# Performance work log

Hardware: AMD Instinct MI355X
Metric: run time of the kernel (lower is better)

## Reference

```python
import jax, jax.numpy as jnp
import numpy as np

DIM = 64

def conv2d_g2(x, w, b):
    # 3x3 conv, padding=1, groups=2, NCHW
    y = jax.lax.conv_general_dilated(x, w, (1, 1), [(1, 1), (1, 1)],
                                     dimension_numbers=('NCHW', 'OIHW', 'NCHW'),
                                     feature_group_count=2)
    return y + b[None, :, None, None]

def bilinear_gather(x, py, px):
    # x: [B,C,H,W]; py,px: [B,K,H,W] float sample coords -> [B,K,H,W,C]
    B, C, H, W = x.shape
    y0 = jnp.floor(py); x0 = jnp.floor(px)
    ly = py - y0; lx = px - x0
    hy = 1.0 - ly; hx = 1.0 - lx
    b_idx = jnp.arange(B)[:, None, None, None]
    def gather(yi, xi):
        valid = (yi >= 0) & (yi < H) & (xi >= 0) & (xi < W)
        yc = jnp.clip(yi, 0, H - 1).astype(jnp.int32)
        xc = jnp.clip(xi, 0, W - 1).astype(jnp.int32)
        v = x[b_idx, :, yc, xc]  # [B,K,H,W,C]
        return v * valid[..., None].astype(x.dtype)
    return (gather(y0, x0) * (hy * hx)[..., None]
            + gather(y0, x0 + 1) * (hy * lx)[..., None]
            + gather(y0 + 1, x0) * (ly * hx)[..., None]
            + gather(y0 + 1, x0 + 1) * (ly * lx)[..., None])

def deform_dw(x, offset, w, b, k, pad, dil):
    # depthwise (groups=C, offset_groups=1) deformable conv, stride 1
    B, C, H, W = x.shape
    K = k * k
    off = offset.reshape(B, K, 2, H, W)  # torchvision layout: (dy,dx) per kernel tap
    ky = jnp.repeat(jnp.arange(k), k).astype(x.dtype)   # [K]
    kx = jnp.tile(jnp.arange(k), k).astype(x.dtype)     # [K]
    base_y = jnp.arange(H, dtype=x.dtype)[None, None, :, None] - pad + dil * ky[None, :, None, None]
    base_x = jnp.arange(W, dtype=x.dtype)[None, None, None, :] - pad + dil * kx[None, :, None, None]
    py = base_y + off[:, :, 0]  # [B,K,H,W]
    px = base_x + off[:, :, 1]
    val = bilinear_gather(x, py, px)  # [B,K,H,W,C]
    return jnp.einsum('bkhwc,ck->bchw', val, w.reshape(C, K)) + b[None, :, None, None]

def lsk_forward(x, w_off3, b_off3, w_off2, b_off2, w7, b7, w5, b5):
    B, C, H, W = x.shape
    offset3 = conv2d_g2(x, w_off3, b_off3)            # [B,98,H,W]
    out1 = deform_dw(x, offset3, w7, b7, 7, 9, 3)     # [B,C,H,W]
    offset2 = conv2d_g2(x, w_off2, b_off2)            # [B,50,H,W]
    out2 = deform_dw(out1, offset2, w5, b5, 5, 6, 3)  # [B,C,H,W]
    feats = jnp.stack([out1, out2], axis=1)           # [B,2,C,H,W]
    gap = feats.mean(axis=(3, 4), keepdims=True)      # [B,2,C,1,1]
    attn = jax.nn.softmax(gap, axis=1)
    return jnp.sum(feats * attn, axis=1)              # [B,C,H,W]

def setup_inputs() -> dict:
    key = jax.random.key(0)
    ks = jax.random.split(key, 9)
    B, C, H, W = 4, DIM, 56, 56
    return {
        'x':      jax.random.normal(ks[0], (B, C, H, W), jnp.float32),
        'w_off3': jax.random.normal(ks[1], (98, C // 2, 3, 3), jnp.float32) * 0.05,
        'b_off3': jax.random.normal(ks[2], (98,), jnp.float32) * 0.05,
        'w_off2': jax.random.normal(ks[3], (50, C // 2, 3, 3), jnp.float32) * 0.05,
        'b_off2': jax.random.normal(ks[4], (50,), jnp.float32) * 0.05,
        'w7':     jax.random.normal(ks[5], (C, 1, 7, 7), jnp.float32) * 0.1,
        'b7':     jax.random.normal(ks[6], (C,), jnp.float32) * 0.05,
        'w5':     jax.random.normal(ks[7], (C, 1, 5, 5), jnp.float32) * 0.1,
        'b5':     jax.random.normal(ks[8], (C,), jnp.float32) * 0.05,
    }

def reference(x, w_off3, b_off3, w_off2, b_off2, w7, b7, w5, b5):
    return lsk_forward(x, w_off3, b_off3, w_off2, b_off2, w7, b7, w5, b5)
```

## Files before the change

### kernel.cpp

```cpp
#include <hip/hip_runtime.h>
#include <hip/hip_fp16.h>
#include <math.h>

#define HH 56
#define WW 56
#define CC 64
#define BB 4
#define HWA (HH*WW)

typedef _Float16 half8_t __attribute__((ext_vector_type(8)));
typedef _Float16 h2_t   __attribute__((ext_vector_type(2)));
typedef float f32x4_t __attribute__((ext_vector_type(4)));

#define PROWS 57
#define PSTRB (PROWS*57*64*4)
#define ROWSTRB (57*64*4)

__global__ __launch_bounds__(256)
void k_prep(const float* __restrict__ x,
            const float* __restrict__ w3, const float* __restrict__ w2,
            const float* __restrict__ b3, const float* __restrict__ b2,
            __half2* __restrict__ xp, _Float16* __restrict__ xh,
            _Float16* __restrict__ Wp, float* __restrict__ bbp) {
    int blk = blockIdx.x;
    int tid = threadIdx.x;
    if (blk < BB*56) {
        __shared__ float ld[64*57];
        int b = blk / 56, y = blk % 56;
        for (int i = tid; i < 64*56; i += 256) {
            int c = i / 56, col = i % 56;
            ld[c*57 + col] = x[((size_t)b*CC + c)*HWA + y*WW + col];
        }
        __syncthreads();
        for (int i = tid; i < 57*64; i += 256) {
            int j = i >> 6, c = i & 63;
            float lo = (j > 0)  ? ld[c*57 + j - 1] : 0.f;
            float hi = (j < 56) ? ld[c*57 + j]     : 0.f;
            xp[((size_t)(b*PROWS + y)*57 + j)*CC + c] = __floats2half2_rn(lo, hi);
        }
        _Float16* dst = xh + (((size_t)(b*2)*56 + y)*58)*32;
        for (int i = tid; i < 2*58*32; i += 256) {
            int g = i / 1856;
            int r = i % 1856;
            int col = r / 32, ic = r % 32;
            float v = 0.f;
            if (col >= 1 && col <= 56) v = ld[(g*32 + ic)*57 + col - 1];
            dst[(size_t)g*56*58*32 + r] = (_Float16)v;
        }
    } else {
        int i = (blk - BB*56)*256 + tid;
        if (i < 46080) {
            int j    = i & 7;
            int lane = (i >> 3) & 63;
            int mt   = (i >> 9) % 5;
            int kt   = (i / 2560) % 9;
            int g    = i / 23040;
            int m  = mt*16 + (lane & 15);
            int ic = (lane >> 4)*8 + j;
            int ky = kt/3, kx = kt%3;
            float v = 0.f;
            if (m < 49)      v = w3[((g*49 + m)*32 + ic)*9 + ky*3 + kx];
            else if (m < 74) v = w2[((g*25 + (m-49))*32 + ic)*9 + ky*3 + kx];
            Wp[i] = (_Float16)v;
        } else if (i < 46240) {
            int t = i - 46080; int g = t/80, m = t%80;
            float v = 0.f;
            if (m < 49)      v = b3[g*49 + m];
            else if (m < 74) v = b2[g*25 + (m-49)];
            bbp[t] = v;
        }
    }
}

__global__ __launch_bounds__(256)
void k_convmfma(const _Float16* __restrict__ xh, const _Float16* __restrict__ Wp,
                const float* __restrict__ bb,
                float* __restrict__ off3, float* __restrict__ off2) {
    __shared__ _Float16 tile[4][3*18*32];
    int blk = blockIdx.x;
    int iy = blk % 56;
    int g  = (blk / 56) & 1;
    int b  = blk / 112;
    int wv   = threadIdx.y;
    int lane = threadIdx.x;
    int n0 = wv * 16;

    const unsigned int* xs = (const unsigned int*)xh;
    unsigned int* tl = (unsigned int*)&tile[wv][0];
#pragma unroll
    for (int i = 0; i < 14; ++i) {
        int idx = i*64 + lane;
        if (idx < 864) {
            int ic2 = idx & 15;
            int seg = idx >> 4;
            int cl = seg % 18, r = seg / 18;
            int y = iy - 1 + r, col = n0 + cl;
            unsigned int v = 0;
            if (y >= 0 && y < 56 && col < 58)
                v = xs[(((size_t)(b*2+g)*56 + y)*58 + col)*16 + ic2];
            tl[idx] = v;
        }
    }
    __syncthreads();

    int nlo = lane & 15, khi = lane >> 4;
    f32x4_t acc[5];
#pragma unroll
    for (int mt = 0; mt < 5; ++mt) acc[mt] = (f32x4_t){0.f,0.f,0.f,0.f};

    const half8_t* wp8 = (const half8_t*)Wp;
#pragma unroll
    for (int kt = 0; kt < 9; ++kt) {
        int ky = kt/3, kx = kt%3;
        half8_t bfrag = *(const half8_t*)&tile[wv][((ky*18) + nlo + kx)*32 + khi*8];
#pragma unroll
        for (int mt = 0; mt < 5; ++mt) {
            half8_t afrag = wp8[(((size_t)g*9 + kt)*5 + mt)*64 + lane];
            acc[mt] = __builtin_amdgcn_mfma_f32_16x16x32_f16(afrag, bfrag, acc[mt], 0, 0, 0);
        }
    }

    int pixcol = n0 + nlo;
    if (pixcol < 56) {
        int pix = iy*WW + pixcol;
#pragma unroll
        for (int mt = 0; mt < 5; ++mt) {
#pragma unroll
            for (int r = 0; r < 4; ++r) {
                int m = mt*16 + khi*4 + r;
                if (m < 74) {
                    float val = acc[mt][r] + bb[g*80 + m];
                    if (m < 49)
                        off3[((size_t)b*98 + g*49 + m)*HWA + pix] = val;
                    else
                        off2[((size_t)b*50 + g*25 + (m-49))*HWA + pix] = val;
                }
            }
        }
    }
}

template<int K, int KS, int PAD, bool WP>
__global__ __launch_bounds__(256)
void k_deform(const _Float16* __restrict__ xp, const float* __restrict__ off,
              const float* __restrict__ wg, const float* __restrict__ bias,
              float* __restrict__ out, float* __restrict__ partial,
              _Float16* __restrict__ xpo) {
    __shared__ float lw[K*65];
    __shared__ float loffs[2*K][9];
    __shared__ float red[8][64];
    int tid = threadIdx.x + threadIdx.y*64;
    int blk = blockIdx.x;
    int xcd = blk & 7;
    int idx = blk >> 3;
    int b   = xcd >> 1;
    int hw0 = (xcd & 1)*(HWA/2) + idx*8;

    for (int i = tid; i < K*64; i += 256) {
        int c = i / K, t = i % K;
        lw[t*65 + c] = wg[i];
    }
    for (int i = tid; i < 4*K; i += 256) {
        int row = i >> 1, half = i & 1;
        float4 v = *(const float4*)&off[((size_t)b*2*K + row)*HWA + hw0 + half*4];
        loffs[row][half*4 + 0] = v.x; loffs[row][half*4 + 1] = v.y;
        loffs[row][half*4 + 2] = v.z; loffs[row][half*4 + 3] = v.w;
    }
    __syncthreads();

    int yp = threadIdx.y;
    int c  = threadIdx.x;

    int mx0 = 0, wz0 = 0, ww0 = 0;
    int mx1 = 0, wz1 = 0, ww1 = 0;
    if (c < K) {
        int t = c;
        int ky = t / KS, kx = t % KS;
#pragma unroll
        for (int s = 0; s < 2; ++s) {
            int p = yp + 4*s;
            int hw = hw0 + p;
            int h = hw / WW, w = hw % WW;
            float py = (float)(h - PAD + 3*ky) + loffs[2*t][p];
            float px = (float)(w - PAD + 3*kx) + loffs[2*t+1][p];
            float y0f = floorf(py), x0f = floorf(px);
            float ly = py - y0f, lx = px - x0f;
            float hy = 1.f - ly, hx = 1.f - lx;
            int y0 = (int)y0f, x0 = (int)x0f;
            int j = x0 + 1;
            bool jv = (j >= 0) && (j <= 56);
            int jc = jv ? j : 0;
            float s0 = ((y0   >= 0) && (y0   < HH) && jv) ? hy : 0.f;
            float s1 = ((y0+1 >= 0) && (y0+1 < HH) && jv) ? ly : 0.f;
            bool use1 = (s0 == 0.f);
            int rbase = use1 ? min(max(y0 + 1, 0), 55) : y0;
            float aw = use1 ? s1 : s0;
            float bw = use1 ? 0.f : s1;
            int mxv = (rbase*57 + jc)*(64*4);
            __half2 wah = __floats2half2_rn(aw*hx, aw*lx);
            __half2 wbh = __floats2half2_rn(bw*hx, bw*lx);
            if (s == 0) { mx0 = mxv; wz0 = *(int*)&wah; ww0 = *(int*)&wbh; }
            else        { mx1 = mxv; wz1 = *(int*)&wah; ww1 = *(int*)&wbh; }
        }
    }

    const char* xb = (const char*)xp + (size_t)b*PSTRB;
    float acc0 = 0.f, acc1 = 0.f;
#pragma unroll 4
    for (int t = 0; t < K; ++t) {
        int m0 = (int)__builtin_amdgcn_readlane(mx0, t);
        int z0 = (int)__builtin_amdgcn_readlane(wz0, t);
        int w0 = (int)__builtin_amdgcn_readlane(ww0, t);
        int m1 = (int)__builtin_amdgcn_readlane(mx1, t);
        int z1 = (int)__builtin_amdgcn_readlane(wz1, t);
        int w1 = (int)__builtin_amdgcn_readlane(ww1, t);
        const h2_t* r0p = (const h2_t*)(xb + m0);
        const h2_t* r1p = (const h2_t*)(xb + m0 + ROWSTRB);
        const h2_t* r2p = (const h2_t*)(xb + m1);
        const h2_t* r3p = (const h2_t*)(xb + m1 + ROWSTRB);
        h2_t r0a = r0p[c];
        h2_t r1a = r1p[c];
        h2_t r0b = r2p[c];
        h2_t r1b = r3p[c];
        float lwv = lw[t*65 + c];
        float v0 = __builtin_amdgcn_fdot2(r0a, *(h2_t*)&z0, 0.f, false);
        v0 = __builtin_amdgcn_fdot2(r1a, *(h2_t*)&w0, v0, false);
        float v1 = __builtin_amdgcn_fdot2(r0b, *(h2_t*)&z1, 0.f, false);
        v1 = __builtin_amdgcn_fdot2(r1b, *(h2_t*)&w1, v1, false);
        acc0 = fmaf(v0, lwv, acc0);
        acc1 = fmaf(v1, lwv, acc1);
    }
    float bs = bias[c];
    float val0 = acc0 + bs;
    float val1 = acc1 + bs;
    int hwA = hw0 + yp, hwB = hw0 + yp + 4;
    out[((size_t)b*HWA + hwA)*CC + c] = val0;
    out[((size_t)b*HWA + hwB)*CC + c] = val1;

    if (WP) {
#pragma unroll
        for (int s = 0; s < 2; ++s) {
            int hw = s ? hwB : hwA;
            float val = s ? val1 : val0;
            int y = hw / WW, w = hw % WW;
            _Float16* base = xpo + ((size_t)(b*PROWS + y)*57)*CC*2;
            _Float16 hv = (_Float16)val;
            base[((w    )*64 + c)*2 + 1] = hv;
            base[((w + 1)*64 + c)*2 + 0] = hv;
            if (w == 0)  base[(c)*2 + 0] = (_Float16)0.f;
            if (w == 55) base[((56)*64 + c)*2 + 1] = (_Float16)0.f;
        }
    }

    red[yp][c] = val0;
    red[yp + 4][c] = val1;
    __syncthreads();
    if (yp == 0) {
        float s = red[0][c] + red[1][c] + red[2][c] + red[3][c]
                + red[4][c] + red[5][c] + red[6][c] + red[7][c];
        partial[((size_t)b*(HWA/8) + (hw0 >> 3))*64 + c] = s;
    }
}

__global__ void k_gapA(const float* __restrict__ p1, const float* __restrict__ p2,
                       float* __restrict__ g2) {
    __shared__ float red[4][64];
    int blk = blockIdx.x;
    int chunk = blk % 14;
    int bf    = blk / 14;
    int b     = bf >> 1;
    const float* p = (bf & 1) ? p2 : p1;
    int tid = threadIdx.x;
    int c = tid & 63, s = tid >> 6;
    float sum = 0.f;
#pragma unroll
    for (int i = 0; i < 7; ++i) {
        int j = chunk*28 + s + 4*i;
        sum += p[((size_t)b*(HWA/8) + j)*64 + c];
    }
    red[s][c] = sum;
    __syncthreads();
    if (s == 0)
        g2[((size_t)bf*14 + chunk)*64 + c]
            = red[0][c] + red[1][c] + red[2][c] + red[3][c];
}

__global__ void k_combine(const float* __restrict__ o1, const float* __restrict__ o2,
                          const float* __restrict__ g2, float* __restrict__ out) {
    __shared__ float tile[64][65];
    __shared__ float gsh[2][64];
    int blk = blockIdx.x;
    int b   = blk / (HWA/64);
    int t0  = (blk % (HWA/64)) * 64;
    int tid = threadIdx.x;
    int c = tid & 63, q = tid >> 6;

    if (tid < 128) {
        int f = tid >> 6, cc = tid & 63;
        float s = 0.f;
#pragma unroll
        for (int k = 0; k < 14; ++k)
            s += g2[((size_t)(b*2+f)*14 + k)*64 + cc];
        gsh[f][cc] = s * (1.f/HWA);
    }
    __syncthreads();

    float g1v = gsh[0][c];
    float g2v = gsh[1][c];
    float m  = fmaxf(g1v, g2v);
    float e1 = expf(g1v - m), e2 = expf(g2v - m);
    float a1 = e1 / (e1 + e2), a2 = 1.f - a1;

#pragma unroll
    for (int i = 0; i < 16; ++i) {
        int p = q + 4*i;
        size_t idx = ((size_t)b*HWA + t0 + p)*CC + c;
        tile[p][c] = o1[idx]*a1 + o2[idx]*a2;
    }
    __syncthreads();
    int p2 = tid & 63;
#pragma unroll
    for (int i = 0; i < 16; ++i) {
        int c2 = q + 4*i;
        out[((size_t)b*CC + c2)*HWA + t0 + p2] = tile[p2][c2];
    }
}

extern "C" void kernel_launch(void* const* d_in, const int* in_sizes, int n_in,
                              void* d_out, int out_size, void* d_ws, size_t ws_size,
                              hipStream_t stream) {
    const float* x      = (const float*)d_in[0];
    const float* w_off3 = (const float*)d_in[1];
    const float* b_off3 = (const float*)d_in[2];
    const float* w_off2 = (const float*)d_in[3];
    const float* b_off2 = (const float*)d_in[4];
    const float* w7     = (const float*)d_in[5];
    const float* b7     = (const float*)d_in[6];
    const float* w5     = (const float*)d_in[7];
    const float* b5     = (const float*)d_in[8];
    float* out = (float*)d_out;

    const size_t PAIRF = (size_t)BB*PROWS*57*64;
    float* ws    = (float*)d_ws;
    float* off3r = ws;
    float* off2r = off3r + 1229312;
    float* out1  = off2r + 627200;
    float* out2  = out1  + 802816;
    float* xp1f  = out2  + 802816;
    float* xp2f  = xp1f  + PAIRF;
    float* xhf   = xp2f  + PAIRF;
    float* part1 = xhf   + 415744;
    float* part2 = part1 + 100352;
    float* gpA   = part2 + 100352;
    float* wpf   = gpA   + 7168;
    float* bbp   = wpf   + 23040;
    __half2*  xp1 = (__half2*)xp1f;
    _Float16* xp2h = (_Float16*)xp2f;
    _Float16* xh  = (_Float16*)xhf;
    _Float16* Wp  = (_Float16*)wpf;
    size_t need = (size_t)(1229312 + 627200 + 802816*2 + 831744*2 + 415744
                           + 100352*2 + 7168 + 23040 + 160) * 4;
    if (ws_size < need) return;

    k_prep<<<BB*56 + 181, 256, 0, stream>>>(x, w_off3, w_off2, b_off3, b_off2,
                                            xp1, xh, Wp, bbp);
    k_convmfma<<<BB*2*56, dim3(64,4), 0, stream>>>(xh, Wp, bbp, off3r, off2r);
    k_deform<49,7,9,true><<<BB*(HWA/8), dim3(64,4), 0, stream>>>(
        (const _Float16*)xp1, off3r, w7, b7, out1, part1, xp2h);
    k_deform<25,5,6,false><<<BB*(HWA/8), dim3(64,4), 0, stream>>>(
        xp2h, off2r, w5, b5, out2, part2, nullptr);
    k_gapA<<<8*14, 256, 0, stream>>>(part1, part2, gpA);
    k_combine<<<BB*(HWA/64), 256, 0, stream>>>(out1, out2, gpA, out);
}
```

Measured before the change: 139.6 us.

## Vectorize conv tile loads and combine reads, deepen deform loop unroll

The MFMA conv kernel now fills its shared tile with 16-byte uint4 loads instead of 4-byte loads. The combine kernel computes the softmax attention weights once per channel and reads o1/o2 as float4. The deformable-conv tap loop is unrolled by 8 instead of 4, and the prep kernel's fp16 repack loop is split per group so it uses shifts instead of div/mod. These changes aim to cut memory instruction count and integer overhead, at the cost of possible register pressure from the deeper unroll and more LDS bank conflicts on the strided tile writes.

After: 135.2 us (median of 3 runs). 1.03x faster.

```diff
diff --git a/kernel.cpp b/kernel.cpp
--- a/kernel.cpp
+++ b/kernel.cpp
@@ -39,13 +39,13 @@
             xp[((size_t)(b*PROWS + y)*57 + j)*CC + c] = __floats2half2_rn(lo, hi);
         }
         _Float16* dst = xh + (((size_t)(b*2)*56 + y)*58)*32;
-        for (int i = tid; i < 2*58*32; i += 256) {
-            int g = i / 1856;
-            int r = i % 1856;
-            int col = r / 32, ic = r % 32;
-            float v = 0.f;
-            if (col >= 1 && col <= 56) v = ld[(g*32 + ic)*57 + col - 1];
-            dst[(size_t)g*56*58*32 + r] = (_Float16)v;
+#pragma unroll
+        for (int g = 0; g < 2; ++g) {
+            for (int i = tid; i < 1856; i += 256) {
+                int col = i >> 5, ic = i & 31;
+                float v = (col >= 1 && col <= 56) ? ld[(g*32 + ic)*57 + col - 1] : 0.f;
+                dst[(size_t)g*(56*58*32) + i] = (_Float16)v;
+            }
         }
     } else {
         int i = (blk - BB*56)*256 + tid;
@@ -85,20 +85,20 @@
     int lane = threadIdx.x;
     int n0 = wv * 16;
 
-    const unsigned int* xs = (const unsigned int*)xh;
-    unsigned int* tl = (unsigned int*)&tile[wv][0];
-#pragma unroll
-    for (int i = 0; i < 14; ++i) {
-        int idx = i*64 + lane;
-        if (idx < 864) {
-            int ic2 = idx & 15;
-            int seg = idx >> 4;
+    const uint4* xs4 = (const uint4*)xh;
+    uint4* tl4 = (uint4*)&tile[wv][0];
+#pragma unroll
+    for (int i = 0; i < 4; ++i) {
+        int idx4 = i*64 + lane;
+        if (idx4 < 216) {
+            int ic4 = idx4 & 3;
+            int seg = idx4 >> 2;
             int cl = seg % 18, r = seg / 18;
             int y = iy - 1 + r, col = n0 + cl;
-            unsigned int v = 0;
+            uint4 v = {0u, 0u, 0u, 0u};
             if (y >= 0 && y < 56 && col < 58)
-                v = xs[(((size_t)(b*2+g)*56 + y)*58 + col)*16 + ic2];
-            tl[idx] = v;
+                v = xs4[((((size_t)(b*2+g)*56 + y)*58 + col) << 2) + ic4];
+            tl4[idx4] = v;
         }
     }
     __syncthreads();
@@ -206,7 +206,7 @@
 
     const char* xb = (const char*)xp + (size_t)b*PSTRB;
     float acc0 = 0.f, acc1 = 0.f;
-#pragma unroll 4
+#pragma unroll 8
     for (int t = 0; t < K; ++t) {
         int m0 = (int)__builtin_amdgcn_readlane(mx0, t);
         int z0 = (int)__builtin_amdgcn_readlane(wz0, t);
@@ -288,37 +288,47 @@
 __global__ void k_combine(const float* __restrict__ o1, const float* __restrict__ o2,
                           const float* __restrict__ g2, float* __restrict__ out) {
     __shared__ float tile[64][65];
-    __shared__ float gsh[2][64];
+    __shared__ float ash[2][64];
     int blk = blockIdx.x;
     int b   = blk / (HWA/64);
     int t0  = (blk % (HWA/64)) * 64;
     int tid = threadIdx.x;
-    int c = tid & 63, q = tid >> 6;
-
-    if (tid < 128) {
-        int f = tid >> 6, cc = tid & 63;
-        float s = 0.f;
-#pragma unroll
-        for (int k = 0; k < 14; ++k)
-            s += g2[((size_t)(b*2+f)*14 + k)*64 + cc];
-        gsh[f][cc] = s * (1.f/HWA);
-    }
-    __syncthreads();
-
-    float g1v = gsh[0][c];
-    float g2v = gsh[1][c];
-    float m  = fmaxf(g1v, g2v);
-    float e1 = expf(g1v - m), e2 = expf(g2v - m);
-    float a1 = e1 / (e1 + e2), a2 = 1.f - a1;
-
-#pragma unroll
-    for (int i = 0; i < 16; ++i) {
-        int p = q + 4*i;
-        size_t idx = ((size_t)b*HWA + t0 + p)*CC + c;
-        tile[p][c] = o1[idx]*a1 + o2[idx]*a2;
-    }
-    __syncthreads();
-    int p2 = tid & 63;
+
+    if (tid < 64) {
+        int cc = tid;
+        float s1 = 0.f, s2 = 0.f;
+#pragma unroll
+        for (int k = 0; k < 14; ++k) {
+            s1 += g2[((size_t)(b*2+0)*14 + k)*64 + cc];
+            s2 += g2[((size_t)(b*2+1)*14 + k)*64 + cc];
+        }
+        s1 *= (1.f/HWA); s2 *= (1.f/HWA);
+        float m  = fmaxf(s1, s2);
+        float e1 = expf(s1 - m), e2 = expf(s2 - m);
+        float a1 = e1 / (e1 + e2);
+        ash[0][cc] = a1;
+        ash[1][cc] = 1.f - a1;
+    }
+    __syncthreads();
+
+    const float4* o14 = (const float4*)o1;
+    const float4* o24 = (const float4*)o2;
+#pragma unroll
+    for (int i = 0; i < 4; ++i) {
+        int f = i*256 + tid;
+        int p = f >> 4, c4 = f & 15;
+        size_t idx4 = (((size_t)b*HWA + t0 + p)*CC >> 2) + c4;
+        float4 v1 = o14[idx4];
+        float4 v2 = o24[idx4];
+        float4 a1 = *(const float4*)&ash[0][c4*4];
+        float4 a2 = *(const float4*)&ash[1][c4*4];
+        tile[p][c4*4 + 0] = v1.x*a1.x + v2.x*a2.x;
+        tile[p][c4*4 + 1] = v1.y*a1.y + v2.y*a2.y;
+        tile[p][c4*4 + 2] = v1.z*a1.z + v2.z*a2.z;
+        tile[p][c4*4 + 3] = v1.w*a1.w + v2.w*a2.w;
+    }
+    __syncthreads();
+    int q = tid >> 6, p2 = tid & 63;
 #pragma unroll
     for (int i = 0; i < 16; ++i) {
         int c2 = q + 4*i;
```
